# Kernel tuning notes

Measured on AMD Instinct MI355X. Metric: run time of the kernel, lower is better.

## Reference

```python
import jax, jax.numpy as jnp
import numpy as np

B, C, H, W = 32, 384, 56, 56  # batch, channels, spatial; meta_kernel_size == H


def setup_inputs() -> dict:
    key = jax.random.key(0)
    k1, k2, k3 = jax.random.split(key, 3)
    x = jax.random.normal(k1, (B, C, H, W), dtype=jnp.float32)
    # depthwise conv weight: [dim, 1, meta_kernel_size, 1] (OIHW, I = in_ch/groups = 1)
    weight = jax.random.normal(k2, (C, 1, H, 1), dtype=jnp.float32) * 0.02
    bias = jax.random.normal(k3, (C,), dtype=jnp.float32)
    return {"x": x, "weight": weight, "bias": bias}


def reference(x, weight, bias):
    # circular padding along H: cat(x, x[:, :, :-1, :]) -> [B, C, 2H-1, W]
    x_cat = jnp.concatenate([x, x[:, :, :-1, :]], axis=2)
    # depthwise (groups = C) valid conv with full-height kernel -> [B, C, H, W]
    out = jax.lax.conv_general_dilated(
        x_cat, weight,
        window_strides=(1, 1), padding='VALID',
        dimension_numbers=('NCHW', 'OIHW', 'NCHW'),
        feature_group_count=x.shape[1],
    )
    return out + bias[None, :, None, None]
```

## Files before the change

kernel.cpp:

```cpp
#include <hip/hip_runtime.h>

#define NB 32
#define NC 384
#define NH 56
#define NW 56
#define HP 64

typedef __attribute__((ext_vector_type(8))) short  bf16x8;
typedef __attribute__((ext_vector_type(4))) float  f32x4;
typedef __attribute__((ext_vector_type(4))) unsigned int u32x4;

__device__ __forceinline__ unsigned short f2bf(float f) {
    unsigned u = __float_as_uint(f);
    return (unsigned short)((u + 0x7FFFu + ((u >> 16) & 1u)) >> 16);
}

__global__ __launch_bounds__(256, 4) void gcc_Conv2d_64347200028713_kernel(
    const float* __restrict__ x,
    const float* __restrict__ wgt,
    const float* __restrict__ bias,
    float* __restrict__ out)
{
    const int tid  = threadIdx.x;
    const int lane = tid & 63;
    const int wave = tid >> 6;
    const int c    = blockIdx.x >> 3;
    const int g    = blockIdx.x & 7;
    const int b    = g * 4 + wave;
    const int plane = b * NC + c;

    __shared__ float wsh[NH];
    __shared__ __align__(16) unsigned short Mw[HP * HP];
    __shared__ __align__(16) unsigned short Xw_all[4][HP * HP];

    if (tid < NH) wsh[tid] = wgt[c * NH + tid];
    __syncthreads();
#pragma unroll
    for (int i = tid; i < HP * HP; i += 256) {
        const int h = i >> 6, j = i & 63;
        unsigned short v = 0;
        if (h < NH && j < NH) { int d = j - h; if (d < 0) d += NH; v = f2bf(wsh[d]); }
        Mw[i] = v;
    }
    __syncthreads();

    unsigned short* Xw = Xw_all[wave];
    const float* __restrict__ xp = x + (size_t)plane * (NH * NW);

    {
        u32x4 z = {0u, 0u, 0u, 0u};
        *reinterpret_cast<u32x4*>(&Xw[NH * HP + lane * 8]) = z;
    }
    if (lane < 56) {
        const int jin = lane / 14;
        const int wq  = lane % 14;
#pragma unroll
        for (int it = 0; it < 14; ++it) {
            const int j = it * 4 + jin;
            const float4 v = *reinterpret_cast<const float4*>(xp + j * NW + wq * 4);
            const unsigned lo = (unsigned)f2bf(v.x) | ((unsigned)f2bf(v.y) << 16);
            const unsigned hi = (unsigned)f2bf(v.z) | ((unsigned)f2bf(v.w) << 16);
            const unsigned long long pk = ((unsigned long long)hi << 32) | lo;
            *reinterpret_cast<unsigned long long*>(&Xw[j * HP + wq * 4]) = pk;
        }
    }

    const int l15 = lane & 15;
    const int kg  = lane >> 4;
    const float bc = bias[c];
    float* __restrict__ op = out + (size_t)plane * (NH * NW);

#pragma unroll
    for (int half = 0; half < 2; ++half) {
        f32x4 acc[4][2] = {};
#pragma unroll
        for (int kk = 0; kk < 2; ++kk) {
            bf16x8 af[4];
#pragma unroll
            for (int ht = 0; ht < 4; ++ht)
                af[ht] = *reinterpret_cast<const bf16x8*>(
                    &Mw[(ht * 16 + l15) * HP + kk * 32 + kg * 8]);
#pragma unroll
            for (int wtl = 0; wtl < 2; ++wtl) {
                const int n = (half * 2 + wtl) * 16 + l15;
                bf16x8 bf;
#pragma unroll
                for (int e = 0; e < 8; ++e)
                    bf[e] = (short)Xw[(kk * 32 + kg * 8 + e) * HP + n];
#pragma unroll
                for (int ht = 0; ht < 4; ++ht)
                    acc[ht][wtl] = __builtin_amdgcn_mfma_f32_16x16x32_bf16(
                        af[ht], bf, acc[ht][wtl], 0, 0, 0);
            }
        }
#pragma unroll
        for (int ht = 0; ht < 4; ++ht) {
#pragma unroll
            for (int wtl = 0; wtl < 2; ++wtl) {
                const int ww = (half * 2 + wtl) * 16 + l15;
#pragma unroll
                for (int r = 0; r < 4; ++r) {
                    const int hh = ht * 16 + kg * 4 + r;
                    if (hh < NH && ww < NW)
                        op[hh * NW + ww] = acc[ht][wtl][r] + bc;
                }
            }
        }
    }
}

extern "C" void kernel_launch(void* const* d_in, const int* in_sizes, int n_in,
                              void* d_out, int out_size, void* d_ws, size_t ws_size,
                              hipStream_t stream)
{
    const float* x    = (const float*)d_in[0];
    const float* wgt  = (const float*)d_in[1];
    const float* bias = (const float*)d_in[2];
    float* out        = (float*)d_out;

    const int grid  = NC * 8;
    const int block = 256;

    gcc_Conv2d_64347200028713_kernel<<<grid, block, 0, stream>>>(x, wgt, bias, out);
}
```

Before: 304.0 us.

## Load B fragments directly from global memory and swizzle the weight matrix in LDS

Removes the per-wave LDS staging buffer for the input plane. Each lane now loads its B-fragment elements straight from global memory and converts them to bf16 in registers, clamping indices so padded rows and columns read valid memory. The circulant weight matrix in LDS gets an XOR swizzle to reduce bank conflicts, and its A fragments are loaded once and reused across both halves. Launch bounds drop from 4 to 3 blocks per CU, and the LDS footprint shrinks, at the cost of narrow strided scalar global loads instead of float4 loads.

```diff
diff --git a/kernel.cpp b/kernel.cpp
--- a/kernel.cpp
+++ b/kernel.cpp
@@ -8,14 +8,13 @@
 
 typedef __attribute__((ext_vector_type(8))) short  bf16x8;
 typedef __attribute__((ext_vector_type(4))) float  f32x4;
-typedef __attribute__((ext_vector_type(4))) unsigned int u32x4;
 
 __device__ __forceinline__ unsigned short f2bf(float f) {
     unsigned u = __float_as_uint(f);
     return (unsigned short)((u + 0x7FFFu + ((u >> 16) & 1u)) >> 16);
 }
 
-__global__ __launch_bounds__(256, 4) void gcc_Conv2d_64347200028713_kernel(
+__global__ __launch_bounds__(256, 3) void gcc_Conv2d_64347200028713_kernel(
     const float* __restrict__ x,
     const float* __restrict__ wgt,
     const float* __restrict__ bias,
@@ -27,11 +26,10 @@
     const int c    = blockIdx.x >> 3;
     const int g    = blockIdx.x & 7;
     const int b    = g * 4 + wave;
-    const int plane = b * NC + c;
+    const size_t plane = (size_t)(b * NC + c);
 
     __shared__ float wsh[NH];
     __shared__ __align__(16) unsigned short Mw[HP * HP];
-    __shared__ __align__(16) unsigned short Xw_all[4][HP * HP];
 
     if (tid < NH) wsh[tid] = wgt[c * NH + tid];
     __syncthreads();
@@ -40,57 +38,50 @@
         const int h = i >> 6, j = i & 63;
         unsigned short v = 0;
         if (h < NH && j < NH) { int d = j - h; if (d < 0) d += NH; v = f2bf(wsh[d]); }
-        Mw[i] = v;
+        Mw[(h << 6) | (j ^ ((h & 7) << 3))] = v;
     }
     __syncthreads();
 
-    unsigned short* Xw = Xw_all[wave];
-    const float* __restrict__ xp = x + (size_t)plane * (NH * NW);
+    const int l15 = lane & 15;
+    const int kg  = lane >> 4;
+    const float* __restrict__ xp = x   + plane * (NH * NW);
+    float*       __restrict__ op = out + plane * (NH * NW);
+    const float bc = bias[c];
 
-    {
-        u32x4 z = {0u, 0u, 0u, 0u};
-        *reinterpret_cast<u32x4*>(&Xw[NH * HP + lane * 8]) = z;
-    }
-    if (lane < 56) {
-        const int jin = lane / 14;
-        const int wq  = lane % 14;
+    bf16x8 af[4][2];
 #pragma unroll
-        for (int it = 0; it < 14; ++it) {
-            const int j = it * 4 + jin;
-            const float4 v = *reinterpret_cast<const float4*>(xp + j * NW + wq * 4);
-            const unsigned lo = (unsigned)f2bf(v.x) | ((unsigned)f2bf(v.y) << 16);
-            const unsigned hi = (unsigned)f2bf(v.z) | ((unsigned)f2bf(v.w) << 16);
-            const unsigned long long pk = ((unsigned long long)hi << 32) | lo;
-            *reinterpret_cast<unsigned long long*>(&Xw[j * HP + wq * 4]) = pk;
+    for (int ht = 0; ht < 4; ++ht) {
+        const int row = ht * 16 + l15;
+#pragma unroll
+        for (int kk = 0; kk < 2; ++kk) {
+            const int idx = (row << 6) | ((kk * 32 + kg * 8) ^ ((row & 7) << 3));
+            af[ht][kk] = *reinterpret_cast<const bf16x8*>(&Mw[idx]);
         }
     }
-
-    const int l15 = lane & 15;
-    const int kg  = lane >> 4;
-    const float bc = bias[c];
-    float* __restrict__ op = out + (size_t)plane * (NH * NW);
 
 #pragma unroll
     for (int half = 0; half < 2; ++half) {
         f32x4 acc[4][2] = {};
 #pragma unroll
         for (int kk = 0; kk < 2; ++kk) {
-            bf16x8 af[4];
-#pragma unroll
-            for (int ht = 0; ht < 4; ++ht)
-                af[ht] = *reinterpret_cast<const bf16x8*>(
-                    &Mw[(ht * 16 + l15) * HP + kk * 32 + kg * 8]);
+            int j0 = kk * 32 + kg * 8;
+            if (j0 > 48) j0 = 48;
+            bf16x8 bf[2];
 #pragma unroll
             for (int wtl = 0; wtl < 2; ++wtl) {
-                const int n = (half * 2 + wtl) * 16 + l15;
-                bf16x8 bf;
+                int n = (half * 2 + wtl) * 16 + l15;
+                if (n > 55) n = 55;
+                const float* bp = xp + j0 * NW + n;
 #pragma unroll
                 for (int e = 0; e < 8; ++e)
-                    bf[e] = (short)Xw[(kk * 32 + kg * 8 + e) * HP + n];
+                    bf[wtl][e] = (short)f2bf(bp[e * NW]);
+            }
 #pragma unroll
-                for (int ht = 0; ht < 4; ++ht)
+            for (int ht = 0; ht < 4; ++ht) {
+#pragma unroll
+                for (int wtl = 0; wtl < 2; ++wtl)
                     acc[ht][wtl] = __builtin_amdgcn_mfma_f32_16x16x32_bf16(
-                        af[ht], bf, acc[ht][wtl], 0, 0, 0);
+                        af[ht][kk], bf[wtl], acc[ht][wtl], 0, 0, 0);
             }
         }
 #pragma unroll
@@ -98,11 +89,13 @@
 #pragma unroll
             for (int wtl = 0; wtl < 2; ++wtl) {
                 const int ww = (half * 2 + wtl) * 16 + l15;
+                if (ww < NW) {
 #pragma unroll
-                for (int r = 0; r < 4; ++r) {
-                    const int hh = ht * 16 + kg * 4 + r;
-                    if (hh < NH && ww < NW)
-                        op[hh * NW + ww] = acc[ht][wtl][r] + bc;
+                    for (int r = 0; r < 4; ++r) {
+                        const int hh = ht * 16 + kg * 4 + r;
+                        if (hh < NH)
+                            op[hh * NW + ww] = acc[ht][wtl][r] + bc;
+                    }
                 }
             }
         }
```

Result: slower. 341.3 us (+12.3%).
